# Optimization experiments

Hardware: AMD Instinct MI355X
Metric: run time of the kernel (lower is better)

Reference implementation:

```python
import jax, jax.numpy as jnp
import numpy as np

VOCAB = 100000
EMBED = 300
HIDDEN = 300
BATCH = 32768
K_NEG = 10
N_CLASSES = 2
EPS = 1e-5
DENO_W = 1.0
CONO_W = 1.0


def setup_inputs() -> dict:
    key = jax.random.key(0)
    ks = jax.random.split(key, 12)
    init_range = 1.0 / EMBED
    return {
        "center_word_ids": jax.random.randint(ks[0], (BATCH,), 0, VOCAB),
        "context_word_ids": jax.random.randint(ks[1], (BATCH,), 0, VOCAB),
        "neg_context_ids": jax.random.randint(ks[2], (BATCH, K_NEG), 0, VOCAB),
        "party_label": jax.random.randint(ks[3], (BATCH,), 0, N_CLASSES),
        "center_emb": jax.random.uniform(ks[4], (VOCAB, EMBED), jnp.float32, -init_range, init_range),
        "context_emb": jax.random.normal(ks[5], (VOCAB, EMBED), jnp.float32) * 0.02,
        "W_enc": jax.random.normal(ks[6], (HIDDEN, EMBED), jnp.float32) * (1.0 / np.sqrt(EMBED)),
        "b_enc": jnp.zeros((HIDDEN,), jnp.float32),
        "W_dec": jax.random.normal(ks[7], (EMBED, HIDDEN), jnp.float32) * (1.0 / np.sqrt(HIDDEN)),
        "b_dec": jnp.zeros((EMBED,), jnp.float32),
        "W_cls": jax.random.normal(ks[8], (N_CLASSES, HIDDEN), jnp.float32) * (1.0 / np.sqrt(HIDDEN)),
        "b_cls": jnp.zeros((N_CLASSES,), jnp.float32),
    }


def reference(center_word_ids, context_word_ids, neg_context_ids, party_label,
              center_emb, context_emb, W_enc, b_enc, W_dec, b_dec, W_cls, b_cls):
    # encoder_forward (dropout p=0 -> identity)
    emb = center_emb[center_word_ids]                      # [B, E]
    enc = emb @ W_enc.T + b_enc                            # [B, H]
    # deno_forward: skip-gram negative sampling
    center_v = enc @ W_dec.T + b_dec                       # [B, E]
    ctx_v = context_emb[context_word_ids]                  # [B, E]
    pos_score = jnp.clip(jnp.sum(center_v * ctx_v, axis=1), -10.0, 10.0)
    pos = -jax.nn.log_sigmoid(pos_score)                   # [B]
    neg_v = context_emb[neg_context_ids]                   # [B, K, E]
    neg_score = jnp.clip(jnp.einsum('bke,be->bk', neg_v, center_v), -10.0, 10.0)
    neg = -jnp.sum(jax.nn.log_sigmoid(-neg_score), axis=1)  # [B]
    deno_loss = jnp.clip(jnp.mean(pos + neg), EPS, 10.0)
    # cono_forward + cross entropy
    logits = enc @ W_cls.T + b_cls                         # [B, C]
    logp = jax.nn.log_softmax(logits, axis=-1)
    nll = -jnp.take_along_axis(logp, party_label[:, None], axis=1)[:, 0]
    cono_loss = jnp.clip(jnp.mean(nll), EPS, 10.0)
    encoder_loss = jnp.clip(DENO_W * deno_loss + CONO_W * cono_loss, EPS, None)
    return jnp.stack([encoder_loss, deno_loss, cono_loss])
```

## Files before the change

### kernel.cpp

```cpp
#include <hip/hip_runtime.h>
#include <math.h>

#define VOCAB   100000
#define EMBED   300
#define HIDDEN  300
#define BATCH   32768
#define K_NEG   10
#define EPSV    1e-5f

#define KPAD    320
#define NPAD    384
#define CV_STRIDE 304
#define NBUCKET 512

typedef __attribute__((ext_vector_type(8))) short  short8;
typedef __attribute__((ext_vector_type(4))) float  f32x4;

__device__ inline float b2f(unsigned short u) {
    union { unsigned int i; float f; } v; v.i = ((unsigned int)u) << 16; return v.f;
}
__device__ inline unsigned short f2b(float f) {
    union { float f; unsigned int i; } v; v.f = f;
    unsigned int r = v.i + 0x7FFFu + ((v.i >> 16) & 1u);
    return (unsigned short)(r >> 16);
}
__device__ inline float wave_red(float v) {
    #pragma unroll
    for (int o = 32; o; o >>= 1) v += __shfl_down(v, o);
    return v;
}
__device__ inline float softplusf(float x) {
    return x > 0.f ? x + log1pf(expf(-x)) : log1pf(expf(x));
}
__device__ inline float4 bf4(ushort4 u) {
    return make_float4(b2f(u.x), b2f(u.y), b2f(u.z), b2f(u.w));
}
__device__ inline float dot4(float4 a, float4 b, float s) {
    s = fmaf(a.x, b.x, s); s = fmaf(a.y, b.y, s);
    s = fmaf(a.z, b.z, s); s = fmaf(a.w, b.w, s);
    return s;
}
__device__ inline void up2(unsigned int u, float& lo, float& hi) {
    union { unsigned int i; float f; } a, b;
    a.i = u << 16; b.i = u & 0xFFFF0000u;
    lo = a.f; hi = b.f;
}

__global__ __launch_bounds__(256)
void pack_w_kernel(const float* __restrict__ W0, const float* __restrict__ W1,
                   unsigned short* __restrict__ P0, unsigned short* __restrict__ P1)
{
    const int gid = blockIdx.x * 256 + threadIdx.x;
    const int mat = gid / (NPAD * 40);
    const int rem = gid - mat * (NPAD * 40);
    const int r   = rem / 40;
    const int c8  = (rem - r * 40) * 8;
    const float* src = mat ? W1 : W0;
    unsigned short* dst = mat ? P1 : P0;

    unsigned short t[8];
    #pragma unroll
    for (int j = 0; j < 8; ++j) {
        const int c = c8 + j;
        t[j] = (r < 300 && c < 300) ? f2b(src[r * 300 + c]) : (unsigned short)0;
    }
    *(uint4*)(dst + (size_t)r * KPAD + c8) = *(const uint4*)t;
}

__global__ __launch_bounds__(256)
void pack_emb_kernel(const float* __restrict__ emb, const int* __restrict__ ids,
                     unsigned short* __restrict__ out)
{
    const int gid = blockIdx.x * 256 + threadIdx.x;
    const int row = gid / 40;
    const int c8  = (gid - row * 40) * 8;
    const int id  = ids[row];
    const float* src = emb + (size_t)id * 300;

    unsigned short t[8];
    if (c8 + 7 < 300) {
        float4 a = *(const float4*)(src + c8);
        float4 b = *(const float4*)(src + c8 + 4);
        t[0]=f2b(a.x); t[1]=f2b(a.y); t[2]=f2b(a.z); t[3]=f2b(a.w);
        t[4]=f2b(b.x); t[5]=f2b(b.y); t[6]=f2b(b.z); t[7]=f2b(b.w);
    } else {
        #pragma unroll
        for (int j = 0; j < 8; ++j) {
            const int c = c8 + j;
            t[j] = (c < 300) ? f2b(src[c]) : (unsigned short)0;
        }
    }
    *(uint4*)(out + (size_t)row * KPAD + c8) = *(const uint4*)t;
}

__global__ __launch_bounds__(256)
void pack_ctx_kernel(const float* __restrict__ x, unsigned short* __restrict__ out)
{
    const int gid = blockIdx.x * 256 + threadIdx.x;
    if (gid >= VOCAB * 38) return;
    const int row = gid / 38;
    const int c8  = (gid - row * 38) * 8;
    const float* src = x + (size_t)row * 300;

    unsigned short t[8];
    if (c8 + 7 < 300) {
        float4 a = *(const float4*)(src + c8);
        float4 b = *(const float4*)(src + c8 + 4);
        t[0]=f2b(a.x); t[1]=f2b(a.y); t[2]=f2b(a.z); t[3]=f2b(a.w);
        t[4]=f2b(b.x); t[5]=f2b(b.y); t[6]=f2b(b.z); t[7]=f2b(b.w);
    } else {
        #pragma unroll
        for (int j = 0; j < 8; ++j) {
            const int c = c8 + j;
            t[j] = (c < 300) ? f2b(src[c]) : (unsigned short)0;
        }
    }
    *(uint4*)(out + (size_t)row * CV_STRIDE + c8) = *(const uint4*)t;
}

template <int OSTRIDE, bool PAD_ZERO>
__global__ __launch_bounds__(256)
void mfma_gemm_kernel(const unsigned short* __restrict__ A,
                      const unsigned short* __restrict__ B,
                      const float* __restrict__ bias,
                      unsigned short* __restrict__ C)
{
    __shared__ unsigned short As[128][40];
    __shared__ unsigned short Bs[128][40];

    const int tid  = threadIdx.x;
    const int wave = tid >> 6;
    const int lane = tid & 63;
    const int m0 = blockIdx.y * 128;
    const int n0 = blockIdx.x * 128;

    const int wr = (wave & 1) * 64;
    const int wc = (wave >> 1) * 64;
    const int fr = lane & 15;
    const int fq = lane >> 4;

    const int lrow = tid >> 1;
    const int lseg = (tid & 1) * 2;

    f32x4 acc[4][4] = {};

    const unsigned short* aRow = A + (size_t)(m0 + lrow) * KPAD + lseg * 8;
    const unsigned short* bRow = B + (size_t)(n0 + lrow) * KPAD + lseg * 8;

    for (int k0 = 0; k0 < KPAD; k0 += 32) {
        uint4 a0 = *(const uint4*)(aRow + k0);
        uint4 a1 = *(const uint4*)(aRow + k0 + 8);
        uint4 b0 = *(const uint4*)(bRow + k0);
        uint4 b1 = *(const uint4*)(bRow + k0 + 8);
        __syncthreads();
        *(uint4*)&As[lrow][lseg * 8]     = a0;
        *(uint4*)&As[lrow][lseg * 8 + 8] = a1;
        *(uint4*)&Bs[lrow][lseg * 8]     = b0;
        *(uint4*)&Bs[lrow][lseg * 8 + 8] = b1;
        __syncthreads();

        short8 af[4], bfr[4];
        #pragma unroll
        for (int i = 0; i < 4; ++i)
            af[i] = *(const short8*)&As[wr + i * 16 + fr][fq * 8];
        #pragma unroll
        for (int j = 0; j < 4; ++j)
            bfr[j] = *(const short8*)&Bs[wc + j * 16 + fr][fq * 8];
        #pragma unroll
        for (int i = 0; i < 4; ++i)
            #pragma unroll
            for (int j = 0; j < 4; ++j)
                acc[i][j] = __builtin_amdgcn_mfma_f32_16x16x32_bf16(
                    af[i], bfr[j], acc[i][j], 0, 0, 0);
    }

    #pragma unroll
    for (int i = 0; i < 4; ++i) {
        #pragma unroll
        for (int r = 0; r < 4; ++r) {
            const int m = m0 + wr + i * 16 + fq * 4 + r;
            unsigned short* crow = C + (size_t)m * OSTRIDE;
            #pragma unroll
            for (int j = 0; j < 4; ++j) {
                const int n = n0 + wc + j * 16 + fr;
                if (n < 300) {
                    crow[n] = f2b(acc[i][j][r] + bias[n]);
                } else if (PAD_ZERO && n < OSTRIDE) {
                    crow[n] = 0;
                }
            }
        }
    }
}

__global__ __launch_bounds__(256)
void ce_kernel(const unsigned short* __restrict__ encb,
               const int* __restrict__ labels,
               const float* __restrict__ W_cls, const float* __restrict__ b_cls,
               float* __restrict__ cono_buckets)
{
    const int wave = threadIdx.x >> 6;
    const int lane = threadIdx.x & 63;
    const int row  = blockIdx.x * 4 + wave;
    const bool tail = lane < 11;

    __shared__ float blk;
    if (threadIdx.x == 0) blk = 0.f;
    __syncthreads();

    const float4 Z = make_float4(0.f, 0.f, 0.f, 0.f);
    const unsigned short* evp = encb + (size_t)row * KPAD;
    const float4 ev0 = bf4(*(const ushort4*)(evp + 4 * lane));
    const float4 ev1 = tail ? bf4(*(const ushort4*)(evp + 256 + 4 * lane)) : Z;

    const float4 w00 = *(const float4*)(W_cls + 4 * lane);
    const float4 w01 = tail ? *(const float4*)(W_cls + 256 + 4 * lane) : Z;
    const float4 w10 = *(const float4*)(W_cls + 300 + 4 * lane);
    const float4 w11 = tail ? *(const float4*)(W_cls + 300 + 256 + 4 * lane) : Z;

    float p0 = dot4(ev1, w01, dot4(ev0, w00, 0.f));
    float p1 = dot4(ev1, w11, dot4(ev0, w10, 0.f));
    p0 = wave_red(p0); p1 = wave_red(p1);

    if (lane == 0) {
        const float l0 = p0 + b_cls[0];
        const float l1 = p1 + b_cls[1];
        const float mx = fmaxf(l0, l1);
        const float lse = mx + logf(expf(l0 - mx) + expf(l1 - mx));
        const float nll = lse - (labels[row] ? l1 : l0);
        atomicAdd(&blk, nll);
    }
    __syncthreads();
    if (threadIdx.x == 0)
        atomicAdd(&cono_buckets[blockIdx.x & (NBUCKET - 1)], blk);
}

template <bool BF16CTX>
__global__ __launch_bounds__(256)
void score_kernel(const unsigned short* __restrict__ cvb,
                  const int* __restrict__ ctx_ids, const int* __restrict__ neg_ids,
                  const unsigned short* __restrict__ ctxb,
                  const float* __restrict__ ctxf,
                  float* __restrict__ deno_buckets)
{
    const int wave = threadIdx.x >> 6;
    const int lane = threadIdx.x & 63;
    const int unit = blockIdx.x * 4 + wave;
    const int row  = unit / 3;
    const int g    = unit - row * 3;

    __shared__ float blk;
    if (threadIdx.x == 0) blk = 0.f;
    __syncthreads();

    int ids[4];
    const int b = row * K_NEG;
    bool hasPos = false; int nscore = 4;
    if (g == 0) {
        hasPos = true;
        ids[0] = ctx_ids[row];
        ids[1] = neg_ids[b + 0]; ids[2] = neg_ids[b + 1]; ids[3] = neg_ids[b + 2];
    } else if (g == 1) {
        ids[0] = neg_ids[b + 3]; ids[1] = neg_ids[b + 4];
        ids[2] = neg_ids[b + 5]; ids[3] = neg_ids[b + 6];
    } else {
        nscore = 3;
        ids[0] = neg_ids[b + 7]; ids[1] = neg_ids[b + 8];
        ids[2] = neg_ids[b + 9]; ids[3] = neg_ids[b + 9];
    }

    float ds[4];
    const unsigned short* cvp = cvb + (size_t)row * CV_STRIDE;

    if (BF16CTX) {
        const bool act = lane < 38;
        const uint4 zero = make_uint4(0,0,0,0);
        uint4 cvu = act ? *(const uint4*)(cvp + 8 * lane) : zero;
        uint4 gv[4];
        #pragma unroll
        for (int j = 0; j < 4; ++j)
            gv[j] = act ? *(const uint4*)(ctxb + (size_t)ids[j] * CV_STRIDE + 8 * lane)
                        : zero;
        float cvf[8];
        up2(cvu.x, cvf[0], cvf[1]); up2(cvu.y, cvf[2], cvf[3]);
        up2(cvu.z, cvf[4], cvf[5]); up2(cvu.w, cvf[6], cvf[7]);
        #pragma unroll
        for (int j = 0; j < 4; ++j) {
            float gf[8];
            up2(gv[j].x, gf[0], gf[1]); up2(gv[j].y, gf[2], gf[3]);
            up2(gv[j].z, gf[4], gf[5]); up2(gv[j].w, gf[6], gf[7]);
            float s = 0.f;
            #pragma unroll
            for (int e = 0; e < 8; ++e) s = fmaf(cvf[e], gf[e], s);
            ds[j] = s;
        }
    } else {
        const bool act = lane < 75;
        const float4 Z = make_float4(0.f,0.f,0.f,0.f);
        const ushort4 uz = {0,0,0,0};
        float4 cv = bf4(act ? *(const ushort4*)(cvp + 4 * lane) : uz);
        float4 gv[4];
        #pragma unroll
        for (int j = 0; j < 4; ++j)
            gv[j] = act ? *(const float4*)(ctxf + (size_t)ids[j] * 300 + 4 * lane) : Z;
        #pragma unroll
        for (int j = 0; j < 4; ++j) ds[j] = dot4(cv, gv[j], 0.f);
    }

    #pragma unroll
    for (int j = 0; j < 4; ++j) ds[j] = wave_red(ds[j]);

    if (lane == 0) {
        float local = 0.f;
        #pragma unroll
        for (int j = 0; j < 4; ++j) {
            if (j < nscore) {
                float s = fminf(10.f, fmaxf(-10.f, ds[j]));
                local += softplusf((hasPos && j == 0) ? -s : s);
            }
        }
        atomicAdd(&blk, local);
    }
    __syncthreads();
    if (threadIdx.x == 0)
        atomicAdd(&deno_buckets[blockIdx.x & (NBUCKET - 1)], blk);
}

__global__ __launch_bounds__(256)
void finalize_kernel(const float* __restrict__ db, const float* __restrict__ cb,
                     float* __restrict__ out)
{
    const int t = threadIdx.x;
    float d = db[t] + db[t + 256];
    float c = cb[t] + cb[t + 256];
    d = wave_red(d); c = wave_red(c);
    __shared__ float sd[4], sc[4];
    if ((t & 63) == 0) { sd[t >> 6] = d; sc[t >> 6] = c; }
    __syncthreads();
    if (t == 0) {
        const float inv = 1.0f / (float)BATCH;
        float deno = (sd[0] + sd[1] + sd[2] + sd[3]) * inv;
        float cono = (sc[0] + sc[1] + sc[2] + sc[3]) * inv;
        deno = fminf(10.f, fmaxf(EPSV, deno));
        cono = fminf(10.f, fmaxf(EPSV, cono));
        out[0] = fmaxf(EPSV, deno + cono);
        out[1] = deno;
        out[2] = cono;
    }
}

extern "C" void kernel_launch(void* const* d_in, const int* in_sizes, int n_in,
                              void* d_out, int out_size, void* d_ws, size_t ws_size,
                              hipStream_t stream)
{
    const int*   cids  = (const int*)d_in[0];
    const int*   ctx   = (const int*)d_in[1];
    const int*   neg   = (const int*)d_in[2];
    const int*   lab   = (const int*)d_in[3];
    const float* cemb  = (const float*)d_in[4];
    const float* xemb  = (const float*)d_in[5];
    const float* W_enc = (const float*)d_in[6];
    const float* b_enc = (const float*)d_in[7];
    const float* W_dec = (const float*)d_in[8];
    const float* b_dec = (const float*)d_in[9];
    const float* W_cls = (const float*)d_in[10];
    const float* b_cls = (const float*)d_in[11];
    float* out = (float*)d_out;

    unsigned short* emb_b  = (unsigned short*)d_ws;
    unsigned short* wenc_b = emb_b  + (size_t)BATCH * KPAD;
    unsigned short* wdec_b = wenc_b + (size_t)NPAD * KPAD;
    unsigned short* enc_b  = wdec_b + (size_t)NPAD * KPAD;
    unsigned short* cv_b   = enc_b  + (size_t)BATCH * KPAD;
    unsigned short* ctx_b  = cv_b   + (size_t)BATCH * CV_STRIDE;
    float* buckets = (float*)(ctx_b + (size_t)VOCAB * CV_STRIDE);
    const size_t need = (char*)(buckets + 2 * NBUCKET) - (char*)d_ws;
    const bool bf16ctx = ws_size >= need;
    if (!bf16ctx)
        buckets = (float*)(cv_b + (size_t)BATCH * CV_STRIDE);
    float* db = buckets;
    float* cb = buckets + NBUCKET;

    hipMemsetAsync(buckets, 0, 2 * NBUCKET * sizeof(float), stream);

    pack_w_kernel<<<(2 * NPAD * 40) / 256, 256, 0, stream>>>(W_enc, W_dec, wenc_b, wdec_b);
    pack_emb_kernel<<<(BATCH * 40) / 256, 256, 0, stream>>>(cemb, cids, emb_b);
    if (bf16ctx)
        pack_ctx_kernel<<<(VOCAB * 38 + 255) / 256, 256, 0, stream>>>(xemb, ctx_b);

    dim3 ggrid(3, BATCH / 128);
    mfma_gemm_kernel<KPAD, true><<<ggrid, 256, 0, stream>>>(emb_b, wenc_b, b_enc, enc_b);
    mfma_gemm_kernel<CV_STRIDE, true><<<ggrid, 256, 0, stream>>>(enc_b, wdec_b, b_dec, cv_b);

    ce_kernel<<<BATCH / 4, 256, 0, stream>>>(enc_b, lab, W_cls, b_cls, cb);

    const int units = 3 * BATCH;
    if (bf16ctx)
        score_kernel<true><<<units / 4, 256, 0, stream>>>(cv_b, ctx, neg, ctx_b, nullptr, db);
    else
        score_kernel<false><<<units / 4, 256, 0, stream>>>(cv_b, ctx, neg, nullptr, xemb, db);

    finalize_kernel<<<1, 256, 0, stream>>>(db, cb, out);
}
```

Baseline: 424.8 us.

## Pack context table to scaled FP8, fuse prep and score/CE kernels, async LDS loads

The context embedding table is now converted to scaled FP8 instead of bf16, which halves the bytes written during packing and read during the gather in scoring. The three pack kernels are merged into one prep launch, and the CE and score kernels are merged into one kernel with one block per row. The GEMM stages tiles through global_load_lds with a swizzled LDS layout instead of register round-trips. The fallback path for a small workspace is removed, and FP8 lowers the precision of the context vectors, which may shift the loss.

```diff
diff --git a/kernel.cpp b/kernel.cpp
--- a/kernel.cpp
+++ b/kernel.cpp
@@ -8,13 +8,23 @@
 #define K_NEG   10
 #define EPSV    1e-5f
 
-#define KPAD    320
-#define NPAD    384
+#define KPAD      320
+#define NPAD      384
 #define CV_STRIDE 304
+#define CTX8_STRIDE 304
+#define FP8_SCALE 64.0f
+#define FP8_DESCALE 0.015625f
 #define NBUCKET 512
 
 typedef __attribute__((ext_vector_type(8))) short  short8;
 typedef __attribute__((ext_vector_type(4))) float  f32x4;
+typedef __attribute__((ext_vector_type(2))) float  floatx2;
+
+#if defined(__has_builtin)
+#if __has_builtin(__builtin_amdgcn_cvt_pk_f32_fp8) && __has_builtin(__builtin_amdgcn_cvt_pk_fp8_f32)
+#define HAVE_CVT_FP8 1
+#endif
+#endif
 
 __device__ inline float b2f(unsigned short u) {
     union { unsigned int i; float f; } v; v.i = ((unsigned int)u) << 16; return v.f;
@@ -24,6 +34,11 @@
     unsigned int r = v.i + 0x7FFFu + ((v.i >> 16) & 1u);
     return (unsigned short)(r >> 16);
 }
+__device__ inline void up2(unsigned int u, float& lo, float& hi) {
+    union { unsigned int i; float f; } a, b;
+    a.i = u << 16; b.i = u & 0xFFFF0000u;
+    lo = a.f; hi = b.f;
+}
 __device__ inline float wave_red(float v) {
     #pragma unroll
     for (int o = 32; o; o >>= 1) v += __shfl_down(v, o);
@@ -32,90 +47,129 @@
 __device__ inline float softplusf(float x) {
     return x > 0.f ? x + log1pf(expf(-x)) : log1pf(expf(x));
 }
-__device__ inline float4 bf4(ushort4 u) {
-    return make_float4(b2f(u.x), b2f(u.y), b2f(u.z), b2f(u.w));
-}
-__device__ inline float dot4(float4 a, float4 b, float s) {
-    s = fmaf(a.x, b.x, s); s = fmaf(a.y, b.y, s);
-    s = fmaf(a.z, b.z, s); s = fmaf(a.w, b.w, s);
-    return s;
-}
-__device__ inline void up2(unsigned int u, float& lo, float& hi) {
-    union { unsigned int i; float f; } a, b;
-    a.i = u << 16; b.i = u & 0xFFFF0000u;
-    lo = a.f; hi = b.f;
-}
+
+__device__ inline float fp8_to_f(unsigned int u8) {
+    const unsigned s = (u8 >> 7) & 1, e = (u8 >> 3) & 15, m = u8 & 7;
+    float v;
+    if (e) { union { unsigned i; float f; } b; b.i = ((e + 120u) << 23) | (m << 20); v = b.f; }
+    else v = (float)m * 0.001953125f;
+    return s ? -v : v;
+}
+__device__ inline unsigned char f_to_fp8(float x) {
+    union { float f; unsigned i; } b; b.f = x;
+    const unsigned s = (b.i >> 31) << 7;
+    const float a = fabsf(x);
+    if (a >= 440.f) return (unsigned char)(s | 0x7E);
+    if (a < 0.015625f) {
+        int m = (int)rintf(a * 512.f);
+        return (unsigned char)(m >= 8 ? (s | 0x08) : (s | (unsigned)m));
+    }
+    unsigned r = (b.i & 0x7FFFFFFFu) + 0x7FFFFu + ((b.i >> 20) & 1u);
+    unsigned e8 = (r >> 23) - 120u;
+    unsigned m8 = (r >> 20) & 7u;
+    if (e8 > 15u) return (unsigned char)(s | 0x7E);
+    return (unsigned char)(s | (e8 << 3) | m8);
+}
+__device__ inline unsigned enc4fp8(float a, float b, float c, float d) {
+#ifdef HAVE_CVT_FP8
+    int v = 0;
+    v = __builtin_amdgcn_cvt_pk_fp8_f32(a, b, v, false);
+    v = __builtin_amdgcn_cvt_pk_fp8_f32(c, d, v, true);
+    return (unsigned)v;
+#else
+    return (unsigned)f_to_fp8(a) | ((unsigned)f_to_fp8(b) << 8) |
+           ((unsigned)f_to_fp8(c) << 16) | ((unsigned)f_to_fp8(d) << 24);
+#endif
+}
+__device__ inline void dec4fp8(unsigned u, float* f) {
+#ifdef HAVE_CVT_FP8
+    floatx2 lo = __builtin_amdgcn_cvt_pk_f32_fp8((int)u, false);
+    floatx2 hi = __builtin_amdgcn_cvt_pk_f32_fp8((int)u, true);
+    f[0] = lo[0]; f[1] = lo[1]; f[2] = hi[0]; f[3] = hi[1];
+#else
+    f[0] = fp8_to_f(u); f[1] = fp8_to_f(u >> 8);
+    f[2] = fp8_to_f(u >> 16); f[3] = fp8_to_f(u >> 24);
+#endif
+}
+
+__device__ inline void load_lds16(const void* g, void* l) {
+    __builtin_amdgcn_global_load_lds(
+        (const __attribute__((address_space(1))) unsigned int*)g,
+        (__attribute__((address_space(3))) unsigned int*)l, 16, 0, 0);
+}
+
+#define NW (2 * NPAD * 40)
+#define NE (BATCH * 40)
+#define NC (VOCAB * 19)
 
 __global__ __launch_bounds__(256)
-void pack_w_kernel(const float* __restrict__ W0, const float* __restrict__ W1,
-                   unsigned short* __restrict__ P0, unsigned short* __restrict__ P1)
+void prep_kernel(const float* __restrict__ W_enc, const float* __restrict__ W_dec,
+                 const float* __restrict__ cemb, const int* __restrict__ cids,
+                 const float* __restrict__ xemb,
+                 unsigned short* __restrict__ wenc_b, unsigned short* __restrict__ wdec_b,
+                 unsigned short* __restrict__ emb_b, unsigned char* __restrict__ ctx8)
 {
     const int gid = blockIdx.x * 256 + threadIdx.x;
-    const int mat = gid / (NPAD * 40);
-    const int rem = gid - mat * (NPAD * 40);
-    const int r   = rem / 40;
-    const int c8  = (rem - r * 40) * 8;
-    const float* src = mat ? W1 : W0;
-    unsigned short* dst = mat ? P1 : P0;
-
-    unsigned short t[8];
-    #pragma unroll
-    for (int j = 0; j < 8; ++j) {
-        const int c = c8 + j;
-        t[j] = (r < 300 && c < 300) ? f2b(src[r * 300 + c]) : (unsigned short)0;
-    }
-    *(uint4*)(dst + (size_t)r * KPAD + c8) = *(const uint4*)t;
-}
-
-__global__ __launch_bounds__(256)
-void pack_emb_kernel(const float* __restrict__ emb, const int* __restrict__ ids,
-                     unsigned short* __restrict__ out)
-{
-    const int gid = blockIdx.x * 256 + threadIdx.x;
-    const int row = gid / 40;
-    const int c8  = (gid - row * 40) * 8;
-    const int id  = ids[row];
-    const float* src = emb + (size_t)id * 300;
-
-    unsigned short t[8];
-    if (c8 + 7 < 300) {
-        float4 a = *(const float4*)(src + c8);
-        float4 b = *(const float4*)(src + c8 + 4);
-        t[0]=f2b(a.x); t[1]=f2b(a.y); t[2]=f2b(a.z); t[3]=f2b(a.w);
-        t[4]=f2b(b.x); t[5]=f2b(b.y); t[6]=f2b(b.z); t[7]=f2b(b.w);
-    } else {
+    if (gid < NW) {
+        const int mat = gid / (NPAD * 40);
+        const int rem = gid - mat * (NPAD * 40);
+        const int r   = rem / 40;
+        const int c8  = (rem - r * 40) * 8;
+        const float* src = mat ? W_dec : W_enc;
+        unsigned short* dst = mat ? wdec_b : wenc_b;
+        unsigned short t[8];
         #pragma unroll
         for (int j = 0; j < 8; ++j) {
             const int c = c8 + j;
-            t[j] = (c < 300) ? f2b(src[c]) : (unsigned short)0;
-        }
-    }
-    *(uint4*)(out + (size_t)row * KPAD + c8) = *(const uint4*)t;
-}
-
-__global__ __launch_bounds__(256)
-void pack_ctx_kernel(const float* __restrict__ x, unsigned short* __restrict__ out)
-{
-    const int gid = blockIdx.x * 256 + threadIdx.x;
-    if (gid >= VOCAB * 38) return;
-    const int row = gid / 38;
-    const int c8  = (gid - row * 38) * 8;
-    const float* src = x + (size_t)row * 300;
-
-    unsigned short t[8];
-    if (c8 + 7 < 300) {
-        float4 a = *(const float4*)(src + c8);
-        float4 b = *(const float4*)(src + c8 + 4);
-        t[0]=f2b(a.x); t[1]=f2b(a.y); t[2]=f2b(a.z); t[3]=f2b(a.w);
-        t[4]=f2b(b.x); t[5]=f2b(b.y); t[6]=f2b(b.z); t[7]=f2b(b.w);
-    } else {
-        #pragma unroll
-        for (int j = 0; j < 8; ++j) {
-            const int c = c8 + j;
-            t[j] = (c < 300) ? f2b(src[c]) : (unsigned short)0;
-        }
-    }
-    *(uint4*)(out + (size_t)row * CV_STRIDE + c8) = *(const uint4*)t;
+            t[j] = (r < 300 && c < 300) ? f2b(src[r * 300 + c]) : (unsigned short)0;
+        }
+        *(uint4*)(dst + (size_t)r * KPAD + c8) = *(const uint4*)t;
+    } else if (gid < NW + NE) {
+        const int g2  = gid - NW;
+        const int row = g2 / 40;
+        const int c8  = (g2 - row * 40) * 8;
+        const float* src = cemb + (size_t)cids[row] * 300;
+        unsigned short t[8];
+        if (c8 + 7 < 300) {
+            float4 a = *(const float4*)(src + c8);
+            float4 b = *(const float4*)(src + c8 + 4);
+            t[0]=f2b(a.x); t[1]=f2b(a.y); t[2]=f2b(a.z); t[3]=f2b(a.w);
+            t[4]=f2b(b.x); t[5]=f2b(b.y); t[6]=f2b(b.z); t[7]=f2b(b.w);
+        } else {
+            #pragma unroll
+            for (int j = 0; j < 8; ++j) {
+                const int c = c8 + j;
+                t[j] = (c < 300) ? f2b(src[c]) : (unsigned short)0;
+            }
+        }
+        *(uint4*)(emb_b + (size_t)row * KPAD + c8) = *(const uint4*)t;
+    } else if (gid < NW + NE + NC) {
+        const int g3  = gid - (NW + NE);
+        const int row = g3 / 19;
+        const int l   = g3 - row * 19;
+        const int e0  = l * 16;
+        const float* src = xemb + (size_t)row * 300 + e0;
+        float v[16];
+        #pragma unroll
+        for (int q = 0; q < 4; ++q) {
+            if (e0 + q * 4 + 3 < 300) {
+                float4 a = *(const float4*)(src + q * 4);
+                v[q*4+0]=a.x; v[q*4+1]=a.y; v[q*4+2]=a.z; v[q*4+3]=a.w;
+            } else {
+                #pragma unroll
+                for (int j = 0; j < 4; ++j) {
+                    const int e = e0 + q * 4 + j;
+                    v[q*4+j] = (e < 300) ? src[q*4+j] : 0.f;
+                }
+            }
+        }
+        unsigned u[4];
+        #pragma unroll
+        for (int q = 0; q < 4; ++q)
+            u[q] = enc4fp8(v[q*4]*FP8_SCALE, v[q*4+1]*FP8_SCALE,
+                           v[q*4+2]*FP8_SCALE, v[q*4+3]*FP8_SCALE);
+        *(uint4*)(ctx8 + (size_t)row * CTX8_STRIDE + e0) = make_uint4(u[0],u[1],u[2],u[3]);
+    }
 }
 
 template <int OSTRIDE, bool PAD_ZERO>
@@ -125,8 +179,8 @@
                       const float* __restrict__ bias,
                       unsigned short* __restrict__ C)
 {
-    __shared__ unsigned short As[128][40];
-    __shared__ unsigned short Bs[128][40];
+    __shared__ unsigned short As[128 * 32];
+    __shared__ unsigned short Bs[128 * 32];
 
     const int tid  = threadIdx.x;
     const int wave = tid >> 6;
@@ -139,39 +193,51 @@
     const int fr = lane & 15;
     const int fq = lane >> 4;
 
-    const int lrow = tid >> 1;
-    const int lseg = (tid & 1) * 2;
+    const unsigned short* gA[2];
+    const unsigned short* gB[2];
+    int ldsOff[2];
+    #pragma unroll
+    for (int inst = 0; inst < 2; ++inst) {
+        const int t = wave * 2 + inst;
+        const int r = (t << 4) + (lane >> 2);
+        const int c = ((lane & 3) - r - (r >> 2)) & 3;
+        gA[inst] = A + (size_t)(m0 + r) * KPAD + c * 8;
+        gB[inst] = B + (size_t)(n0 + r) * KPAD + c * 8;
+        ldsOff[inst] = t << 9;
+    }
+
+    int aoff[4], boff[4];
+    #pragma unroll
+    for (int i = 0; i < 4; ++i) {
+        const int ra = wr + i * 16 + fr;
+        aoff[i] = (ra << 5) + (((fq + ra + (ra >> 2)) & 3) << 3);
+        const int rb = wc + i * 16 + fr;
+        boff[i] = (rb << 5) + (((fq + rb + (rb >> 2)) & 3) << 3);
+    }
 
     f32x4 acc[4][4] = {};
 
-    const unsigned short* aRow = A + (size_t)(m0 + lrow) * KPAD + lseg * 8;
-    const unsigned short* bRow = B + (size_t)(n0 + lrow) * KPAD + lseg * 8;
-
     for (int k0 = 0; k0 < KPAD; k0 += 32) {
-        uint4 a0 = *(const uint4*)(aRow + k0);
-        uint4 a1 = *(const uint4*)(aRow + k0 + 8);
-        uint4 b0 = *(const uint4*)(bRow + k0);
-        uint4 b1 = *(const uint4*)(bRow + k0 + 8);
+        #pragma unroll
+        for (int inst = 0; inst < 2; ++inst) {
+            load_lds16(gA[inst] + k0, As + ldsOff[inst]);
+            load_lds16(gB[inst] + k0, Bs + ldsOff[inst]);
+        }
         __syncthreads();
-        *(uint4*)&As[lrow][lseg * 8]     = a0;
-        *(uint4*)&As[lrow][lseg * 8 + 8] = a1;
-        *(uint4*)&Bs[lrow][lseg * 8]     = b0;
-        *(uint4*)&Bs[lrow][lseg * 8 + 8] = b1;
+
+        short8 af[4], bf[4];
+        #pragma unroll
+        for (int i = 0; i < 4; ++i) af[i] = *(const short8*)&As[aoff[i]];
+        #pragma unroll
+        for (int j = 0; j < 4; ++j) bf[j] = *(const short8*)&Bs[boff[j]];
         __syncthreads();
 
-        short8 af[4], bfr[4];
-        #pragma unroll
-        for (int i = 0; i < 4; ++i)
-            af[i] = *(const short8*)&As[wr + i * 16 + fr][fq * 8];
-        #pragma unroll
-        for (int j = 0; j < 4; ++j)
-            bfr[j] = *(const short8*)&Bs[wc + j * 16 + fr][fq * 8];
         #pragma unroll
         for (int i = 0; i < 4; ++i)
             #pragma unroll
             for (int j = 0; j < 4; ++j)
                 acc[i][j] = __builtin_amdgcn_mfma_f32_16x16x32_bf16(
-                    af[i], bfr[j], acc[i][j], 0, 0, 0);
+                    af[i], bf[j], acc[i][j], 0, 0, 0);
     }
 
     #pragma unroll
@@ -194,136 +260,126 @@
 }
 
 __global__ __launch_bounds__(256)
-void ce_kernel(const unsigned short* __restrict__ encb,
-               const int* __restrict__ labels,
-               const float* __restrict__ W_cls, const float* __restrict__ b_cls,
-               float* __restrict__ cono_buckets)
+void score_ce_kernel(const unsigned short* __restrict__ cvb,
+                     const unsigned short* __restrict__ encb,
+                     const unsigned char* __restrict__ ctx8,
+                     const int* __restrict__ ctx_ids, const int* __restrict__ neg_ids,
+                     const int* __restrict__ labels,
+                     const float* __restrict__ W_cls, const float* __restrict__ b_cls,
+                     float* __restrict__ db, float* __restrict__ cb)
 {
-    const int wave = threadIdx.x >> 6;
+    const int g    = threadIdx.x >> 6;
     const int lane = threadIdx.x & 63;
-    const int row  = blockIdx.x * 4 + wave;
-    const bool tail = lane < 11;
-
-    __shared__ float blk;
-    if (threadIdx.x == 0) blk = 0.f;
+    const int row  = blockIdx.x;
+    const bool act = lane < 19;
+
+    __shared__ float blk[2];
+    if (threadIdx.x < 2) blk[threadIdx.x] = 0.f;
     __syncthreads();
 
-    const float4 Z = make_float4(0.f, 0.f, 0.f, 0.f);
-    const unsigned short* evp = encb + (size_t)row * KPAD;
-    const float4 ev0 = bf4(*(const ushort4*)(evp + 4 * lane));
-    const float4 ev1 = tail ? bf4(*(const ushort4*)(evp + 256 + 4 * lane)) : Z;
-
-    const float4 w00 = *(const float4*)(W_cls + 4 * lane);
-    const float4 w01 = tail ? *(const float4*)(W_cls + 256 + 4 * lane) : Z;
-    const float4 w10 = *(const float4*)(W_cls + 300 + 4 * lane);
-    const float4 w11 = tail ? *(const float4*)(W_cls + 300 + 256 + 4 * lane) : Z;
-
-    float p0 = dot4(ev1, w01, dot4(ev0, w00, 0.f));
-    float p1 = dot4(ev1, w11, dot4(ev0, w10, 0.f));
-    p0 = wave_red(p0); p1 = wave_red(p1);
-
-    if (lane == 0) {
-        const float l0 = p0 + b_cls[0];
-        const float l1 = p1 + b_cls[1];
-        const float mx = fmaxf(l0, l1);
-        const float lse = mx + logf(expf(l0 - mx) + expf(l1 - mx));
-        const float nll = lse - (labels[row] ? l1 : l0);
-        atomicAdd(&blk, nll);
-    }
-    __syncthreads();
-    if (threadIdx.x == 0)
-        atomicAdd(&cono_buckets[blockIdx.x & (NBUCKET - 1)], blk);
-}
-
-template <bool BF16CTX>
-__global__ __launch_bounds__(256)
-void score_kernel(const unsigned short* __restrict__ cvb,
-                  const int* __restrict__ ctx_ids, const int* __restrict__ neg_ids,
-                  const unsigned short* __restrict__ ctxb,
-                  const float* __restrict__ ctxf,
-                  float* __restrict__ deno_buckets)
-{
-    const int wave = threadIdx.x >> 6;
-    const int lane = threadIdx.x & 63;
-    const int unit = blockIdx.x * 4 + wave;
-    const int row  = unit / 3;
-    const int g    = unit - row * 3;
-
-    __shared__ float blk;
-    if (threadIdx.x == 0) blk = 0.f;
-    __syncthreads();
-
-    int ids[4];
-    const int b = row * K_NEG;
-    bool hasPos = false; int nscore = 4;
-    if (g == 0) {
-        hasPos = true;
-        ids[0] = ctx_ids[row];
-        ids[1] = neg_ids[b + 0]; ids[2] = neg_ids[b + 1]; ids[3] = neg_ids[b + 2];
-    } else if (g == 1) {
-        ids[0] = neg_ids[b + 3]; ids[1] = neg_ids[b + 4];
-        ids[2] = neg_ids[b + 5]; ids[3] = neg_ids[b + 6];
-    } else {
-        nscore = 3;
-        ids[0] = neg_ids[b + 7]; ids[1] = neg_ids[b + 8];
-        ids[2] = neg_ids[b + 9]; ids[3] = neg_ids[b + 9];
-    }
-
-    float ds[4];
-    const unsigned short* cvp = cvb + (size_t)row * CV_STRIDE;
-
-    if (BF16CTX) {
-        const bool act = lane < 38;
-        const uint4 zero = make_uint4(0,0,0,0);
-        uint4 cvu = act ? *(const uint4*)(cvp + 8 * lane) : zero;
+    const uint4 Z4 = make_uint4(0, 0, 0, 0);
+
+    if (g < 3) {
+        int ids[4]; int nsc; bool hasPos = false;
+        const int b = row * K_NEG;
+        if (g == 0) {
+            hasPos = true; nsc = 4;
+            ids[0] = ctx_ids[row];
+            ids[1] = neg_ids[b+0]; ids[2] = neg_ids[b+1]; ids[3] = neg_ids[b+2];
+        } else if (g == 1) {
+            nsc = 4;
+            ids[0] = neg_ids[b+3]; ids[1] = neg_ids[b+4];
+            ids[2] = neg_ids[b+5]; ids[3] = neg_ids[b+6];
+        } else {
+            nsc = 3;
+            ids[0] = neg_ids[b+7]; ids[1] = neg_ids[b+8];
+            ids[2] = neg_ids[b+9]; ids[3] = neg_ids[b+9];
+        }
+
+        const char* cvp = (const char*)(cvb + (size_t)row * CV_STRIDE);
+        uint4 c0 = act ? *(const uint4*)(cvp + lane * 32)      : Z4;
+        uint4 c1 = act ? *(const uint4*)(cvp + lane * 32 + 16) : Z4;
+
         uint4 gv[4];
         #pragma unroll
         for (int j = 0; j < 4; ++j)
-            gv[j] = act ? *(const uint4*)(ctxb + (size_t)ids[j] * CV_STRIDE + 8 * lane)
-                        : zero;
-        float cvf[8];
-        up2(cvu.x, cvf[0], cvf[1]); up2(cvu.y, cvf[2], cvf[3]);
-        up2(cvu.z, cvf[4], cvf[5]); up2(cvu.w, cvf[6], cvf[7]);
+            gv[j] = act ? *(const uint4*)(ctx8 + (size_t)ids[j] * CTX8_STRIDE + lane * 16)
+                        : Z4;
+
+        float cvf[16];
+        up2(c0.x, cvf[0], cvf[1]);  up2(c0.y, cvf[2], cvf[3]);
+        up2(c0.z, cvf[4], cvf[5]);  up2(c0.w, cvf[6], cvf[7]);
+        up2(c1.x, cvf[8], cvf[9]);  up2(c1.y, cvf[10], cvf[11]);
+        up2(c1.z, cvf[12], cvf[13]);up2(c1.w, cvf[14], cvf[15]);
+
+        float ds[4];
         #pragma unroll
         for (int j = 0; j < 4; ++j) {
-            float gf[8];
-            up2(gv[j].x, gf[0], gf[1]); up2(gv[j].y, gf[2], gf[3]);
-            up2(gv[j].z, gf[4], gf[5]); up2(gv[j].w, gf[6], gf[7]);
+            float gf[16];
+            dec4fp8(gv[j].x, gf); dec4fp8(gv[j].y, gf + 4);
+            dec4fp8(gv[j].z, gf + 8); dec4fp8(gv[j].w, gf + 12);
             float s = 0.f;
             #pragma unroll
-            for (int e = 0; e < 8; ++e) s = fmaf(cvf[e], gf[e], s);
+            for (int e = 0; e < 16; ++e) s = fmaf(cvf[e], gf[e], s);
             ds[j] = s;
         }
+        #pragma unroll
+        for (int j = 0; j < 4; ++j) ds[j] = wave_red(ds[j]);
+
+        if (lane == 0) {
+            float local = 0.f;
+            #pragma unroll
+            for (int j = 0; j < 4; ++j) {
+                if (j < nsc) {
+                    float s = fminf(10.f, fmaxf(-10.f, ds[j] * FP8_DESCALE));
+                    local += softplusf((hasPos && j == 0) ? -s : s);
+                }
+            }
+            atomicAdd(&blk[0], local);
+        }
     } else {
-        const bool act = lane < 75;
-        const float4 Z = make_float4(0.f,0.f,0.f,0.f);
-        const ushort4 uz = {0,0,0,0};
-        float4 cv = bf4(act ? *(const ushort4*)(cvp + 4 * lane) : uz);
-        float4 gv[4];
-        #pragma unroll
-        for (int j = 0; j < 4; ++j)
-            gv[j] = act ? *(const float4*)(ctxf + (size_t)ids[j] * 300 + 4 * lane) : Z;
-        #pragma unroll
-        for (int j = 0; j < 4; ++j) ds[j] = dot4(cv, gv[j], 0.f);
-    }
-
-    #pragma unroll
-    for (int j = 0; j < 4; ++j) ds[j] = wave_red(ds[j]);
-
-    if (lane == 0) {
-        float local = 0.f;
-        #pragma unroll
-        for (int j = 0; j < 4; ++j) {
-            if (j < nscore) {
-                float s = fminf(10.f, fmaxf(-10.f, ds[j]));
-                local += softplusf((hasPos && j == 0) ? -s : s);
+        const char* evp = (const char*)(encb + (size_t)row * KPAD);
+        uint4 e0 = act ? *(const uint4*)(evp + lane * 32)      : Z4;
+        uint4 e1 = act ? *(const uint4*)(evp + lane * 32 + 16) : Z4;
+        float ev[16];
+        up2(e0.x, ev[0], ev[1]);  up2(e0.y, ev[2], ev[3]);
+        up2(e0.z, ev[4], ev[5]);  up2(e0.w, ev[6], ev[7]);
+        up2(e1.x, ev[8], ev[9]);  up2(e1.y, ev[10], ev[11]);
+        up2(e1.z, ev[12], ev[13]);up2(e1.w, ev[14], ev[15]);
+
+        float p0 = 0.f, p1 = 0.f;
+        #pragma unroll
+        for (int q = 0; q < 4; ++q) {
+            const int e = lane * 16 + q * 4;
+            if (e + 3 < 300) {
+                float4 w0 = *(const float4*)(W_cls + e);
+                float4 w1 = *(const float4*)(W_cls + 300 + e);
+                p0 = fmaf(ev[q*4], w0.x, p0); p0 = fmaf(ev[q*4+1], w0.y, p0);
+                p0 = fmaf(ev[q*4+2], w0.z, p0); p0 = fmaf(ev[q*4+3], w0.w, p0);
+                p1 = fmaf(ev[q*4], w1.x, p1); p1 = fmaf(ev[q*4+1], w1.y, p1);
+                p1 = fmaf(ev[q*4+2], w1.z, p1); p1 = fmaf(ev[q*4+3], w1.w, p1);
+            } else {
+                #pragma unroll
+                for (int j = 0; j < 4; ++j) {
+                    if (e + j < 300) {
+                        p0 = fmaf(ev[q*4+j], W_cls[e + j], p0);
+                        p1 = fmaf(ev[q*4+j], W_cls[300 + e + j], p1);
+                    }
+                }
             }
         }
-        atomicAdd(&blk, local);
+        p0 = wave_red(p0); p1 = wave_red(p1);
+        if (lane == 0) {
+            const float l0 = p0 + b_cls[0];
+            const float l1 = p1 + b_cls[1];
+            const float mx = fmaxf(l0, l1);
+            const float lse = mx + logf(expf(l0 - mx) + expf(l1 - mx));
+            blk[1] = lse - (labels[row] ? l1 : l0);
+        }
     }
     __syncthreads();
-    if (threadIdx.x == 0)
-        atomicAdd(&deno_buckets[blockIdx.x & (NBUCKET - 1)], blk);
+    if (threadIdx.x == 0) atomicAdd(&db[blockIdx.x & (NBUCKET - 1)], blk[0]);
+    if (threadIdx.x == 1) atomicAdd(&cb[blockIdx.x & (NBUCKET - 1)], blk[1]);
 }
 
 __global__ __launch_bounds__(256)
@@ -372,33 +428,22 @@
     unsigned short* wdec_b = wenc_b + (size_t)NPAD * KPAD;
     unsigned short* enc_b  = wdec_b + (size_t)NPAD * KPAD;
     unsigned short* cv_b   = enc_b  + (size_t)BATCH * KPAD;
-    unsigned short* ctx_b  = cv_b   + (size_t)BATCH * CV_STRIDE;
-    float* buckets = (float*)(ctx_b + (size_t)VOCAB * CV_STRIDE);
-    const size_t need = (char*)(buckets + 2 * NBUCKET) - (char*)d_ws;
-    const bool bf16ctx = ws_size >= need;
-    if (!bf16ctx)
-        buckets = (float*)(cv_b + (size_t)BATCH * CV_STRIDE);
+    unsigned char*  ctx8   = (unsigned char*)(cv_b + (size_t)BATCH * CV_STRIDE);
+    float* buckets = (float*)(ctx8 + (size_t)VOCAB * CTX8_STRIDE);
     float* db = buckets;
     float* cb = buckets + NBUCKET;
 
     hipMemsetAsync(buckets, 0, 2 * NBUCKET * sizeof(float), stream);
 
-    pack_w_kernel<<<(2 * NPAD * 40) / 256, 256, 0, stream>>>(W_enc, W_dec, wenc_b, wdec_b);
-    pack_emb_kernel<<<(BATCH * 40) / 256, 256, 0, stream>>>(cemb, cids, emb_b);
-    if (bf16ctx)
-        pack_ctx_kernel<<<(VOCAB * 38 + 255) / 256, 256, 0, stream>>>(xemb, ctx_b);
+    const int nprep = (NW + NE + NC + 255) / 256;
+    prep_kernel<<<nprep, 256, 0, stream>>>(W_enc, W_dec, cemb, cids, xemb,
+                                           wenc_b, wdec_b, emb_b, ctx8);
 
     dim3 ggrid(3, BATCH / 128);
     mfma_gemm_kernel<KPAD, true><<<ggrid, 256, 0, stream>>>(emb_b, wenc_b, b_enc, enc_b);
     mfma_gemm_kernel<CV_STRIDE, true><<<ggrid, 256, 0, stream>>>(enc_b, wdec_b, b_dec, cv_b);
 
-    ce_kernel<<<BATCH / 4, 256, 0, stream>>>(enc_b, lab, W_cls, b_cls, cb);
-
-    const int units = 3 * BATCH;
-    if (bf16ctx)
-        score_kernel<true><<<units / 4, 256, 0, stream>>>(cv_b, ctx, neg, ctx_b, nullptr, db);
-    else
-        score_kernel<false><<<units / 4, 256, 0, stream>>>(cv_b, ctx, neg, nullptr, xemb, db);
-
+    score_ce_kernel<<<BATCH, 256, 0, stream>>>(cv_b, enc_b, ctx8, ctx, neg, lab,
+                                               W_cls, b_cls, db, cb);
     finalize_kernel<<<1, 256, 0, stream>>>(db, cb, out);
 }
```

Result: no change. 426.3 us (+0.3%).
